# Performance work log

Hardware: AMD Instinct MI355X
Metric: run time of the kernel (lower is better)

Reference implementation:

```python
import jax, jax.numpy as jnp
import numpy as np

WS = 8          # window_size
HEADS = 3       # num_heads
DIM = 96        # dim
PDIM = 30       # GlobalAttention patch_dim
EPS_G = 1e-8    # GlobalAttention eps
ATT_A, ATT_B = 30.0, 20.0


def _rel_pos_log(ws):
    # matches get_relative_positions (torch.meshgrid default 'ij' indexing)
    coords = np.stack(np.meshgrid(np.arange(ws), np.arange(ws), indexing='ij'))  # (2,ws,ws)
    cf = coords.reshape(2, -1)                                                    # (2,N)
    rel = (cf[:, :, None] - cf[:, None, :]).transpose(1, 2, 0).astype(np.float32)  # (N,N,2)
    return jnp.asarray(np.sign(rel) * np.log1p(np.abs(rel)))


def _conv(x, w, stride=1, pad=0, groups=1):
    return jax.lax.conv_general_dilated(
        x, w, (stride, stride), [(pad, pad), (pad, pad)],
        feature_group_count=groups, dimension_numbers=('NCHW', 'OIHW', 'NCHW'))


def _refpad(x, p):
    return jnp.pad(x, ((0, 0), (0, 0), (p, p), (p, p)), mode='reflect')


def _forward(X, hf_w1, hf_b1, hf_w2, hf_b2, lfv_w, lfv_b, lfqk_w, lfqk_b,
             meta_w1, meta_b1, meta_w2, meta_b2,
             pe_w1, pe_b1, pe_w2, pe_b2, att_alpha, att_beta,
             fus_w1, fus_w2):
    B, C, H, W = X.shape
    # ---- high-frequency branch: two depthwise 5x5 convs, reflect padding ----
    hf = _conv(_refpad(X, 2), hf_w1, groups=C) + hf_b1[None, :, None, None]
    hf = jax.nn.relu(hf)
    hf = _conv(_refpad(hf, 2), hf_w2, groups=C) + hf_b2[None, :, None, None]
    # ---- low-frequency branch: build QKV (note torch cat order [QK, V]) ----
    lf_v = _conv(X, lfv_w) + lfv_b[None, :, None, None]
    lf_qk = _conv(X, lfqk_w) + lfqk_b[None, :, None, None]
    qkv = jnp.concatenate([lf_qk, lf_v], axis=1)          # (B,3C,H,W)
    # shift_size=0, H,W divisible by WS -> check_size is identity
    x = qkv.transpose(0, 2, 3, 1)                          # (B,H,W,3C)
    nh, nw = H // WS, W // WS
    N = WS * WS
    win = x.reshape(B, nh, WS, nw, WS, 3 * C).transpose(0, 1, 3, 2, 4, 5)
    win = win.reshape(-1, N, 3 * C)                        # (Bw,N,3C)
    # ---- WindowAttention with MLP relative-position bias ----
    Bw = win.shape[0]
    hd = C // HEADS
    qkv_ = win.reshape(Bw, N, 3, HEADS, hd).transpose(2, 0, 3, 1, 4)
    q = qkv_[0] * (hd ** -0.5)
    k, v = qkv_[1], qkv_[2]
    attn = jnp.einsum('bhnd,bhmd->bhnm', q, k)
    rel = _rel_pos_log(WS)                                 # (N,N,2)
    bias = jax.nn.relu(rel @ meta_w1.T + meta_b1) @ meta_w2.T + meta_b2  # (N,N,heads)
    attn = jax.nn.softmax(attn + bias.transpose(2, 0, 1)[None], axis=-1)
    aw = jnp.einsum('bhnm,bhmd->bhnd', attn, v).transpose(0, 2, 1, 3).reshape(Bw, N, C)
    # ---- GlobalAttention: patch embed, l2norm, exp-similarity, l1norm, AdaIN ----
    x4 = aw.reshape(B, nh, nw, N * C)
    src_mean = x4.mean(axis=(1, 2, 3), keepdims=True)      # (B,1,1,1)
    src_std = jnp.sqrt(((x4 - src_mean) ** 2).mean(axis=(1, 2, 3), keepdims=True) + EPS_G)
    emb = jax.nn.relu(x4 @ pe_w1.T + pe_b1) @ pe_w2.T + pe_b2
    emb = emb.reshape(B, nh * nw, PDIM)
    emb = emb / (jnp.sqrt((emb ** 2).sum(-1, keepdims=True)) + EPS_G)
    att_g = jnp.einsum('bnd,bmd->bnm', emb, emb)           # (B,P,P)
    att_g = jnp.exp(ATT_A * att_alpha[0] * att_g + ATT_B * att_beta[0])
    att_g = att_g / (att_g.sum(-1, keepdims=True) + EPS_G)
    rw = jnp.einsum('bnm,bmc->bnc', att_g, aw.reshape(B, nh * nw, N * C))
    cur_mean = emb.mean(axis=(1, 2), keepdims=True)        # stats of embedded x, per source
    cur_std = jnp.sqrt(((emb - cur_mean) ** 2).mean(axis=(1, 2), keepdims=True) + EPS_G)
    rw = (rw - cur_mean) / cur_std
    rw = rw * src_std[:, :, :, 0] + src_mean[:, :, :, 0]
    # ---- window reverse (shift_size=0 -> slice is identity) ----
    out = rw.reshape(B, nh, nw, WS, WS, C).transpose(0, 1, 3, 2, 4, 5).reshape(B, H, W, C)
    lf = out.transpose(0, 3, 1, 2)                         # (B,C,H,W)
    # ---- SKFusion (keep_dim=True): sum, conv mlp, channel softmax gate ----
    feats_sum = hf + lf
    a = _conv(feats_sum, fus_w1, stride=2, pad=1)
    a = jax.nn.relu(a)
    a = _conv(a, fus_w2, stride=2, pad=1)
    a = a.mean(axis=(2, 3))                                # adaptive avg pool -> (B,C)
    a = jax.nn.softmax(a, axis=1)[:, :, None, None]
    return feats_sum * a


def setup_inputs() -> dict:
    key = jax.random.key(0)
    ks = jax.random.split(key, 24)
    B, C, H, W = 4, DIM, 256, 256
    d_fuse = max(C // 2, 4)
    psrc = WS * WS * C
    s = 0.02
    n = lambda k, sh: jax.random.normal(k, sh, dtype=jnp.float32) * s
    return {
        'X': jax.random.normal(ks[0], (B, C, H, W), dtype=jnp.float32),
        'hf_w1': n(ks[1], (C, 1, 5, 5)), 'hf_b1': n(ks[2], (C,)),
        'hf_w2': n(ks[3], (C, 1, 5, 5)), 'hf_b2': n(ks[4], (C,)),
        'lfv_w': n(ks[5], (C, C, 1, 1)), 'lfv_b': n(ks[6], (C,)),
        'lfqk_w': n(ks[7], (2 * C, C, 1, 1)), 'lfqk_b': n(ks[8], (2 * C,)),
        'meta_w1': n(ks[9], (256, 2)), 'meta_b1': n(ks[10], (256,)),
        'meta_w2': n(ks[11], (HEADS, 256)), 'meta_b2': n(ks[12], (HEADS,)),
        'pe_w1': n(ks[13], (256, psrc)), 'pe_b1': n(ks[14], (256,)),
        'pe_w2': n(ks[15], (PDIM, 256)), 'pe_b2': n(ks[16], (PDIM,)),
        'att_alpha': jax.random.normal(ks[17], (1,), dtype=jnp.float32) * 0.01,
        'att_beta': jax.random.normal(ks[18], (1,), dtype=jnp.float32) * 0.01,
        'fus_w1': n(ks[19], (d_fuse, C, 3, 3)), 'fus_w2': n(ks[20], (C, d_fuse, 3, 3)),
    }


def reference(X, hf_w1, hf_b1, hf_w2, hf_b2, lfv_w, lfv_b, lfqk_w, lfqk_b,
              meta_w1, meta_b1, meta_w2, meta_b2,
              pe_w1, pe_b1, pe_w2, pe_b2, att_alpha, att_beta,
              fus_w1, fus_w2):
    return _forward(X, hf_w1, hf_b1, hf_w2, hf_b2, lfv_w, lfv_b, lfqk_w, lfqk_b,
                    meta_w1, meta_b1, meta_w2, meta_b2,
                    pe_w1, pe_b1, pe_w2, pe_b2, att_alpha, att_beta,
                    fus_w1, fus_w2)
```

## Files before the change

kernel.cpp:

```cpp
#include <hip/hip_runtime.h>

constexpr int B_ = 4, C_ = 96, H_ = 256, W_ = 256;
constexpr int NWINS = 4096;
constexpr float EPSG = 1e-8f;
constexpr float ATT_Ac = 30.f, ATT_Bc = 20.f;
constexpr float QSCALE = 0.17677669529663687f;
constexpr long long BIG = (long long)B_ * C_ * H_ * W_;

typedef unsigned short u16;
typedef unsigned int u32;
typedef __attribute__((ext_vector_type(8))) __bf16 bf16x8;
typedef __attribute__((ext_vector_type(4))) float f32x4;

#define AS(n) __attribute__((address_space(n)))

__device__ __forceinline__ void gload16(const void* g, void* l) {
  __builtin_amdgcn_global_load_lds((AS(1) void*)g, (AS(3) void*)l, 16, 0, 0);
}

__device__ __forceinline__ u16 f2b(float f) {
  union { float f; u32 i; } x; x.f = f;
  u32 r = (x.i + 0x7fffu + ((x.i >> 16) & 1u)) >> 16;
  return (u16)r;
}
__device__ __forceinline__ float blo(u32 u) { union { u32 i; float f; } x; x.i = u << 16; return x.f; }
__device__ __forceinline__ float bhi(u32 u) { union { u32 i; float f; } x; x.i = u & 0xffff0000u; return x.f; }

__global__ void k_wt(const float* __restrict__ lfqk_w, const float* __restrict__ lfqk_b,
                     const float* __restrict__ lfv_w, const float* __restrict__ lfv_b,
                     float* __restrict__ wt, float* __restrict__ bq) {
  int t = blockIdx.x * 256 + threadIdx.x;
  if (t < 96 * 288) {
    int ic = t / 288, oc = t % 288;
    wt[t] = (oc < 192) ? lfqk_w[oc * 96 + ic] : lfv_w[(oc - 192) * 96 + ic];
  }
  if (t < 288) bq[t] = (t < 192) ? lfqk_b[t] : lfv_b[t - 192];
}

__global__ void k_bias(const float* __restrict__ w1, const float* __restrict__ b1,
                       const float* __restrict__ w2, const float* __restrict__ b2,
                       float* __restrict__ bias) {
  int t = blockIdx.x * 256 + threadIdx.x;
  if (t >= 4096) return;
  int n = t >> 6, m = t & 63;
  float dy = (float)((n >> 3) - (m >> 3));
  float dx = (float)((n & 7) - (m & 7));
  float fy = (dy > 0.f ? 1.f : (dy < 0.f ? -1.f : 0.f)) * log1pf(fabsf(dy));
  float fx = (dx > 0.f ? 1.f : (dx < 0.f ? -1.f : 0.f)) * log1pf(fabsf(dx));
  float o0 = b2[0], o1 = b2[1], o2 = b2[2];
  for (int j = 0; j < 256; ++j) {
    float h = fmaxf(w1[2 * j] * fy + w1[2 * j + 1] * fx + b1[j], 0.f);
    o0 += w2[j] * h; o1 += w2[256 + j] * h; o2 += w2[512 + j] * h;
  }
  bias[t] = o0; bias[4096 + t] = o1; bias[8192 + t] = o2;
}

__global__ void k_cvtw(const float* __restrict__ in, u16* __restrict__ out, int n) {
  int i = (blockIdx.x * 256 + threadIdx.x) * 4;
  if (i < n) {
    float4 v = *(const float4*)(in + i);
    out[i] = f2b(v.x); out[i + 1] = f2b(v.y); out[i + 2] = f2b(v.z); out[i + 3] = f2b(v.w);
  }
}

__global__ __launch_bounds__(256) void k_qkv(const float* __restrict__ X,
                      const float* __restrict__ wt, const float* __restrict__ bq,
                      float* __restrict__ q, float* __restrict__ k, float* __restrict__ v) {
  __shared__ float xw[96][64];
  int win = blockIdx.x;
  int b = win >> 10, wy = (win >> 5) & 31, wx = win & 31;
  int t = threadIdx.x;
  const float* Xb = X + (long long)b * 96 * 65536 + wy * 8 * 256 + wx * 8;
  for (int f = t; f < 6144; f += 256) {
    int ic = f >> 6, p = f & 63;
    xw[ic][p] = Xb[ic * 65536 + (p >> 3) * 256 + (p & 7)];
  }
  __syncthreads();
  int lane = t & 63, quad = t >> 6;
  int nbase = quad * 16;
  for (int ob = 0; ob < 288; ob += 64) {
    int oc = ob + lane;
    if (oc < 288) {
      float acc[16];
#pragma unroll
      for (int i = 0; i < 16; ++i) acc[i] = 0.f;
#pragma unroll 4
      for (int ic = 0; ic < 96; ++ic) {
        float wv = wt[ic * 288 + oc];
        const float4* xr = (const float4*)&xw[ic][nbase];
#pragma unroll
        for (int g = 0; g < 4; ++g) {
          float4 x = xr[g];
          acc[4 * g + 0] += wv * x.x; acc[4 * g + 1] += wv * x.y;
          acc[4 * g + 2] += wv * x.z; acc[4 * g + 3] += wv * x.w;
        }
      }
      float bb = bq[oc];
      int s = oc / 96, c = oc % 96;
      float scale = (s == 0) ? QSCALE : 1.f;
      float* dst = ((s == 0) ? q : (s == 1) ? k : v) + (long long)win * 6144 + c;
#pragma unroll
      for (int i = 0; i < 16; ++i) dst[(nbase + i) * 96] = (acc[i] + bb) * scale;
    }
  }
}

__global__ __launch_bounds__(192) void k_attn(const float* __restrict__ q, const float* __restrict__ kk_,
                       const float* __restrict__ v, const float* __restrict__ bias,
                       u16* __restrict__ awB) {
  __shared__ float kl[3][64][32];
  __shared__ float vl[3][64][32];
  int win = blockIdx.x;
  int t = threadIdx.x;
  long long base = (long long)win * 6144;
  for (int f = t; f < 6144; f += 192) {
    int n = f / 96, c = f % 96, h = c >> 5, d = c & 31;
    kl[h][n][d] = kk_[base + f];
    vl[h][n][d] = v[base + f];
  }
  __syncthreads();
  int h = t >> 6, lane = t & 63;
  float qr[32];
  const float4* qp = (const float4*)(q + base + lane * 96 + h * 32);
#pragma unroll
  for (int i = 0; i < 8; ++i) {
    float4 x = qp[i];
    qr[4 * i] = x.x; qr[4 * i + 1] = x.y; qr[4 * i + 2] = x.z; qr[4 * i + 3] = x.w;
  }
  const float* bh = bias + h * 4096 + lane * 64;
  float s[64];
#pragma unroll
  for (int m = 0; m < 64; ++m) {
    float acc = 0.f;
    const float4* kp = (const float4*)kl[h][m];
#pragma unroll
    for (int i = 0; i < 8; ++i) {
      float4 x = kp[i];
      acc += qr[4 * i] * x.x + qr[4 * i + 1] * x.y + qr[4 * i + 2] * x.z + qr[4 * i + 3] * x.w;
    }
    s[m] = acc + bh[m];
  }
  float mx = -1e30f;
#pragma unroll
  for (int m = 0; m < 64; ++m) mx = fmaxf(mx, s[m]);
  float sum = 0.f;
#pragma unroll
  for (int m = 0; m < 64; ++m) { float p = __expf(s[m] - mx); s[m] = p; sum += p; }
  float inv = 1.f / sum;
  float o[32];
#pragma unroll
  for (int d = 0; d < 32; ++d) o[d] = 0.f;
#pragma unroll
  for (int m = 0; m < 64; ++m) {
    float p = s[m];
    const float4* vp = (const float4*)vl[h][m];
#pragma unroll
    for (int i = 0; i < 8; ++i) {
      float4 x = vp[i];
      o[4 * i] += p * x.x; o[4 * i + 1] += p * x.y; o[4 * i + 2] += p * x.z; o[4 * i + 3] += p * x.w;
    }
  }
  u32 pk[16];
#pragma unroll
  for (int j = 0; j < 16; ++j)
    pk[j] = (u32)f2b(o[2 * j] * inv) | ((u32)f2b(o[2 * j + 1] * inv) << 16);
  u32* op = (u32*)(awB + base + lane * 96 + h * 32);
#pragma unroll
  for (int j = 0; j < 16; ++j) op[j] = pk[j];
}

__global__ __launch_bounds__(256) void k_awT(const u16* __restrict__ awB, u16* __restrict__ awT) {
  __shared__ u16 tile[64][80];
  int f0 = blockIdx.x * 64, p0 = blockIdx.y * 64, b = blockIdx.z;
  int t = threadIdx.x;
  const u16* src = awB + ((long long)b * 1024 + p0) * 6144 + f0;
  int pr = t >> 2, fc = (t & 3) * 16;
  uint4 v0 = *(const uint4*)(src + (long long)pr * 6144 + fc);
  uint4 v1 = *(const uint4*)(src + (long long)pr * 6144 + fc + 8);
  u16 e[16];
  *(uint4*)&e[0] = v0; *(uint4*)&e[8] = v1;
#pragma unroll
  for (int j = 0; j < 16; ++j) tile[fc + j][pr] = e[j];
  __syncthreads();
  int fr = t >> 2, pc = (t & 3) * 16;
  u16* dst = awT + ((long long)b * 6144 + f0 + fr) * 1024 + p0 + pc;
  *(uint4*)(dst) = *(const uint4*)&tile[fr][pc];
  *(uint4*)(dst + 8) = *(const uint4*)&tile[fr][pc + 8];
}

__global__ void k_redA(const u16* __restrict__ awB, float* __restrict__ part) {
  int b = blockIdx.x, blk = blockIdx.y, t = threadIdx.x;
  const uint4* p = (const uint4*)(awB + (long long)b * 6291456 + (long long)blk * 49152);
  float s = 0.f, ss = 0.f;
  for (int i = t; i < 6144; i += 256) {
    uint4 x = p[i];
    u32 w[4] = {x.x, x.y, x.z, x.w};
#pragma unroll
    for (int j = 0; j < 4; ++j) {
      float a = blo(w[j]), c = bhi(w[j]);
      s += a + c; ss += a * a + c * c;
    }
  }
  __shared__ float r1[256], r2[256];
  r1[t] = s; r2[t] = ss; __syncthreads();
  for (int st = 128; st; st >>= 1) {
    if (t < st) { r1[t] += r1[t + st]; r2[t] += r2[t + st]; }
    __syncthreads();
  }
  if (t == 0) { part[(b * 128 + blk) * 2] = r1[0]; part[(b * 128 + blk) * 2 + 1] = r2[0]; }
}

__global__ void k_redB(const float* __restrict__ part, float* __restrict__ stats) {
  int b = blockIdx.x, t = threadIdx.x;
  float s = part[(b * 128 + t) * 2], ss = part[(b * 128 + t) * 2 + 1];
  __shared__ float r1[128], r2[128];
  r1[t] = s; r2[t] = ss; __syncthreads();
  for (int st = 64; st; st >>= 1) {
    if (t < st) { r1[t] += r1[t + st]; r2[t] += r2[t + st]; }
    __syncthreads();
  }
  if (t == 0) {
    float n = 6291456.f, m = r1[0] / n;
    stats[b] = m;
    stats[4 + b] = sqrtf(fmaxf(r2[0] / n - m * m, 0.f) + EPSG);
  }
}

__global__ __launch_bounds__(256) void k_embed1(const u16* __restrict__ awB, const u16* __restrict__ peB,
                         const float* __restrict__ b1, float* __restrict__ hid) {
  __shared__ __align__(16) u16 As[128 * 32];
  __shared__ __align__(16) u16 Bs[64 * 32];
  int n0 = blockIdx.x * 64, m0 = blockIdx.y * 128;
  int t = threadIdx.x;
  const u16* Ag = awB + (long long)m0 * 6144;
  const u16* Bg = peB + (long long)n0 * 6144;
  f32x4 acc[4][2];
  f32x4 z = {0.f, 0.f, 0.f, 0.f};
#pragma unroll
  for (int i = 0; i < 4; ++i) { acc[i][0] = z; acc[i][1] = z; }
  int w = t >> 6, l = t & 63;
  int wm = (w >> 1) * 64, wn = (w & 1) * 32;
  int ro = l & 15, ko = (l >> 4) * 16;
  for (int k0 = 0; k0 < 6144; k0 += 32) {
#pragma unroll
    for (int i = 0; i < 2; ++i) {
      int c = t + 256 * i;
      gload16(Ag + (long long)(c >> 2) * 6144 + k0 + (c & 3) * 8, (char*)As + c * 16);
    }
    gload16(Bg + (long long)(t >> 2) * 6144 + k0 + (t & 3) * 8, (char*)Bs + t * 16);
    __syncthreads();
    bf16x8 a[4], bb[2];
#pragma unroll
    for (int fm = 0; fm < 4; ++fm)
      a[fm] = *(const bf16x8*)((const char*)As + (wm + fm * 16 + ro) * 64 + ko);
#pragma unroll
    for (int fn = 0; fn < 2; ++fn)
      bb[fn] = *(const bf16x8*)((const char*)Bs + (wn + fn * 16 + ro) * 64 + ko);
#pragma unroll
    for (int fm = 0; fm < 4; ++fm)
#pragma unroll
      for (int fn = 0; fn < 2; ++fn)
        acc[fm][fn] = __builtin_amdgcn_mfma_f32_16x16x32_bf16(a[fm], bb[fn], acc[fm][fn], 0, 0, 0);
    __syncthreads();
  }
#pragma unroll
  for (int fm = 0; fm < 4; ++fm)
#pragma unroll
    for (int r = 0; r < 4; ++r) {
      int m = m0 + wm + fm * 16 + (l >> 4) * 4 + r;
#pragma unroll
      for (int fn = 0; fn < 2; ++fn) {
        int n = n0 + wn + fn * 16 + (l & 15);
        hid[(long long)m * 256 + n] = fmaxf(acc[fm][fn][r] + b1[n], 0.f);
      }
    }
}

__global__ __launch_bounds__(64) void k_embed2(const float* __restrict__ hid, const float* __restrict__ w2,
                        const float* __restrict__ b2, float* __restrict__ emb) {
  __shared__ float hrow[256];
  int pa = blockIdx.x, t = threadIdx.x;
  const float* hp = hid + (long long)pa * 256;
  for (int i = t; i < 256; i += 64) hrow[i] = hp[i];
  __syncthreads();
  float acc = 0.f;
  if (t < 30) {
    acc = b2[t];
    const float* wp = w2 + t * 256;
    for (int j = 0; j < 256; ++j) acc += wp[j] * hrow[j];
  }
  float sq = (t < 30) ? acc * acc : 0.f;
  for (int off = 32; off; off >>= 1) sq += __shfl_down(sq, off);
  float ss = __shfl(sq, 0);
  float scale = 1.f / (sqrtf(ss) + EPSG);
  if (t < 30) emb[(long long)pa * 30 + t] = acc * scale;
}

__global__ void k_curstats(const float* __restrict__ emb, float* __restrict__ stats) {
  int b = blockIdx.x, t = threadIdx.x;
  const float* p = emb + (long long)b * 30720;
  float s = 0.f, ss = 0.f;
  for (int i = t; i < 30720; i += 256) { float x = p[i]; s += x; ss += x * x; }
  __shared__ float r1[256], r2[256];
  r1[t] = s; r2[t] = ss; __syncthreads();
  for (int st = 128; st; st >>= 1) {
    if (t < st) { r1[t] += r1[t + st]; r2[t] += r2[t + st]; }
    __syncthreads();
  }
  if (t == 0) {
    float n = 30720.f, m = r1[0] / n;
    stats[8 + b] = m;
    stats[12 + b] = sqrtf(fmaxf(r2[0] / n - m * m, 0.f) + EPSG);
  }
}

__global__ void k_gatt(const float* __restrict__ emb, const float* __restrict__ alpha,
                       const float* __restrict__ beta, u16* __restrict__ attB) {
  __shared__ float er[64][33];
  __shared__ float ec[64][33];
  int b = blockIdx.x, r0 = blockIdx.y * 64, t = threadIdx.x;
  const float* eb = emb + (long long)b * 30720;
  for (int f = t; f < 1920; f += 256) er[f / 30][f % 30] = eb[(r0 + f / 30) * 30 + f % 30];
  float ca = ATT_Ac * alpha[0], cb = ATT_Bc * beta[0];
  int lane = t & 63, w = t >> 6;
  for (int c0 = 0; c0 < 1024; c0 += 64) {
    __syncthreads();
    for (int f = t; f < 1920; f += 256) ec[f / 30][f % 30] = eb[(c0 + f / 30) * 30 + f % 30];
    __syncthreads();
    for (int rr = w; rr < 64; rr += 4) {
      float acc = 0.f;
#pragma unroll
      for (int d = 0; d < 30; ++d) acc += er[rr][d] * ec[lane][d];
      attB[((long long)b * 1024 + r0 + rr) * 1024 + c0 + lane] = f2b(__expf(ca * acc + cb));
    }
  }
}

__global__ void k_rowsum(const u16* __restrict__ attB, float* __restrict__ rowsum) {
  int row = blockIdx.x * 4 + (threadIdx.x >> 6);
  int lane = threadIdx.x & 63;
  const uint4* p = (const uint4*)(attB + (long long)row * 1024);
  float s = 0.f;
  for (int i = lane; i < 128; i += 64) {
    uint4 x = p[i];
    s += blo(x.x) + bhi(x.x) + blo(x.y) + bhi(x.y) + blo(x.z) + bhi(x.z) + blo(x.w) + bhi(x.w);
  }
  for (int off = 32; off; off >>= 1) s += __shfl_down(s, off);
  if (lane == 0) rowsum[row] = s;
}

__global__ __launch_bounds__(256) void k_rw(const u16* __restrict__ attB, const u16* __restrict__ x4T,
                     const float* __restrict__ rowsum, const float* __restrict__ stats,
                     float* __restrict__ rw) {
  __shared__ __align__(16) u16 As[128 * 32];
  __shared__ __align__(16) u16 Bs[128 * 32];
  int b = blockIdx.z;
  int n0 = blockIdx.x * 128, m0 = blockIdx.y * 128;
  const u16* Ag = attB + ((long long)b * 1024 + m0) * 1024;
  const u16* Bg = x4T + ((long long)b * 6144 + n0) * 1024;
  int t = threadIdx.x;
  f32x4 acc[4][4];
  f32x4 z = {0.f, 0.f, 0.f, 0.f};
#pragma unroll
  for (int i = 0; i < 4; ++i)
#pragma unroll
    for (int j = 0; j < 4; ++j) acc[i][j] = z;
  int w = t >> 6, l = t & 63;
  int wm = (w >> 1) * 64, wn = (w & 1) * 64;
  int ro = l & 15, ko = (l >> 4) * 16;
  for (int k0 = 0; k0 < 1024; k0 += 32) {
#pragma unroll
    for (int i = 0; i < 2; ++i) {
      int c = t + 256 * i;
      gload16(Ag + (c >> 2) * 1024 + k0 + (c & 3) * 8, (char*)As + c * 16);
      gload16(Bg + (c >> 2) * 1024 + k0 + (c & 3) * 8, (char*)Bs + c * 16);
    }
    __syncthreads();
    bf16x8 a[4], bb[4];
#pragma unroll
    for (int fm = 0; fm < 4; ++fm)
      a[fm] = *(const bf16x8*)((const char*)As + (wm + fm * 16 + ro) * 64 + ko);
#pragma unroll
    for (int fn = 0; fn < 4; ++fn)
      bb[fn] = *(const bf16x8*)((const char*)Bs + (wn + fn * 16 + ro) * 64 + ko);
#pragma unroll
    for (int fm = 0; fm < 4; ++fm)
#pragma unroll
      for (int fn = 0; fn < 4; ++fn)
        acc[fm][fn] = __builtin_amdgcn_mfma_f32_16x16x32_bf16(a[fm], bb[fn], acc[fm][fn], 0, 0, 0);
    __syncthreads();
  }
  float sm = stats[b], ssd = stats[4 + b], cm = stats[8 + b], inv_cs = 1.f / stats[12 + b];
#pragma unroll
  for (int fm = 0; fm < 4; ++fm)
#pragma unroll
    for (int r = 0; r < 4; ++r) {
      int m = m0 + wm + fm * 16 + (l >> 4) * 4 + r;
      float sc = 1.f / (rowsum[b * 1024 + m] + EPSG);
      float* dst = rw + ((long long)b * 1024 + m) * 6144 + n0 + wn + (l & 15);
#pragma unroll
      for (int fn = 0; fn < 4; ++fn) {
        float val = acc[fm][fn][r] * sc;
        dst[fn * 16] = (val - cm) * inv_cs * ssd + sm;
      }
    }
}

template <bool RELU>
__global__ void k_dwconv(const float* __restrict__ in, const float* __restrict__ w,
                         const float* __restrict__ bias, float* __restrict__ out) {
  int x = blockIdx.x * 64 + threadIdx.x;
  int y = blockIdx.y * 4 + threadIdx.y;
  int bc = blockIdx.z, c = bc % 96;
  const float* ip = in + (long long)bc * 65536;
  const float* wp = w + c * 25;
  float acc = bias[c];
#pragma unroll
  for (int ky = 0; ky < 5; ++ky) {
    int iy = y + ky - 2;
    iy = iy < 0 ? -iy : (iy > 255 ? 510 - iy : iy);
    const float* row = ip + iy * 256;
#pragma unroll
    for (int kx = 0; kx < 5; ++kx) {
      int ix = x + kx - 2;
      ix = ix < 0 ? -ix : (ix > 255 ? 510 - ix : ix);
      acc += wp[ky * 5 + kx] * row[ix];
    }
  }
  out[(long long)bc * 65536 + y * 256 + x] = RELU ? fmaxf(acc, 0.f) : acc;
}

__global__ void k_fs(const float* __restrict__ rw, const float* __restrict__ hf,
                     float* __restrict__ fs) {
  __shared__ float tile[64 * 97];
  int win = blockIdx.x;
  int b = win >> 10, wy = (win >> 5) & 31, wx = win & 31;
  int t = threadIdx.x;
  const float* src = rw + (long long)win * 6144;
  for (int f = t; f < 6144; f += 256) tile[(f / 96) * 97 + f % 96] = src[f];
  __syncthreads();
  long long obase = (long long)b * 96 * 65536;
  for (int f = t; f < 6144; f += 256) {
    int c = f >> 6, p = f & 63;
    long long oidx = obase + (long long)c * 65536 + (wy * 8 + (p >> 3)) * 256 + wx * 8 + (p & 7);
    fs[oidx] = tile[p * 97 + c] + hf[oidx];
  }
}

__global__ void k_conv1(const float* __restrict__ fs, const float* __restrict__ w,
                        float* __restrict__ out) {
  int ox = blockIdx.x * 64 + threadIdx.x;
  int oy = blockIdx.y * 4 + threadIdx.y;
  int z = blockIdx.z, b = z / 6, og = z % 6, oc0 = og * 8;
  const float* ip = fs + (long long)b * 96 * 65536;
  float acc[8] = {};
  for (int ic = 0; ic < 96; ++ic) {
    const float* plane = ip + (long long)ic * 65536;
    float xv[3][3];
#pragma unroll
    for (int ky = 0; ky < 3; ++ky) {
      int iy = 2 * oy + ky - 1;
#pragma unroll
      for (int kx = 0; kx < 3; ++kx) {
        int ix = 2 * ox + kx - 1;
        xv[ky][kx] = (iy >= 0 && iy < 256 && ix >= 0 && ix < 256) ? plane[iy * 256 + ix] : 0.f;
      }
    }
#pragma unroll
    for (int o = 0; o < 8; ++o) {
      const float* wp = w + ((oc0 + o) * 96 + ic) * 9;
      acc[o] += wp[0] * xv[0][0] + wp[1] * xv[0][1] + wp[2] * xv[0][2]
              + wp[3] * xv[1][0] + wp[4] * xv[1][1] + wp[5] * xv[1][2]
              + wp[6] * xv[2][0] + wp[7] * xv[2][1] + wp[8] * xv[2][2];
    }
  }
#pragma unroll
  for (int o = 0; o < 8; ++o)
    out[(((long long)b * 48 + oc0 + o) * 128 + oy) * 128 + ox] = fmaxf(acc[o], 0.f);
}

__global__ void k_conv2pool(const float* __restrict__ c1, const float* __restrict__ w,
                            float* __restrict__ part) {
  int b = blockIdx.x, og = blockIdx.y, split = blockIdx.z, oc0 = og * 8;
  int t = threadIdx.x;
  const float* ip = c1 + (long long)b * 48 * 16384;
  float acc[8] = {};
  for (int pi = 0; pi < 2; ++pi) {
    int p = split * 512 + pi * 256 + t;
    int oy = p >> 6, ox = p & 63;
    for (int ic = 0; ic < 48; ++ic) {
      const float* plane = ip + ic * 16384;
      float xv[3][3];
#pragma unroll
      for (int ky = 0; ky < 3; ++ky) {
        int iy = 2 * oy + ky - 1;
#pragma unroll
        for (int kx = 0; kx < 3; ++kx) {
          int ix = 2 * ox + kx - 1;
          xv[ky][kx] = (iy >= 0 && iy < 128 && ix >= 0 && ix < 128) ? plane[iy * 128 + ix] : 0.f;
        }
      }
#pragma unroll
      for (int o = 0; o < 8; ++o) {
        const float* wp = w + ((oc0 + o) * 48 + ic) * 9;
        acc[o] += wp[0] * xv[0][0] + wp[1] * xv[0][1] + wp[2] * xv[0][2]
                + wp[3] * xv[1][0] + wp[4] * xv[1][1] + wp[5] * xv[1][2]
                + wp[6] * xv[2][0] + wp[7] * xv[2][1] + wp[8] * xv[2][2];
      }
    }
  }
  __shared__ float red[256];
  for (int o = 0; o < 8; ++o) {
    red[t] = acc[o]; __syncthreads();
    for (int st = 128; st; st >>= 1) {
      if (t < st) red[t] += red[t + st];
      __syncthreads();
    }
    if (t == 0) part[((b * 12 + og) * 8 + split) * 8 + o] = red[0];
    __syncthreads();
  }
}

__global__ void k_gate(const float* __restrict__ part, float* __restrict__ gate) {
  int b = blockIdx.x, t = threadIdx.x;
  __shared__ float val[96];
  __shared__ float red[128];
  if (t < 96) {
    int og = t / 8, o = t % 8;
    float s = 0.f;
    for (int sp = 0; sp < 8; ++sp) s += part[((b * 12 + og) * 8 + sp) * 8 + o];
    val[t] = s / 4096.f;
  }
  __syncthreads();
  float m = (t < 96) ? val[t] : -1e30f;
  red[t] = m; __syncthreads();
  for (int st = 64; st; st >>= 1) { if (t < st) red[t] = fmaxf(red[t], red[t + st]); __syncthreads(); }
  float mx = red[0]; __syncthreads();
  float e = (t < 96) ? __expf(val[t] - mx) : 0.f;
  red[t] = e; __syncthreads();
  for (int st = 64; st; st >>= 1) { if (t < st) red[t] += red[t + st]; __syncthreads(); }
  if (t < 96) gate[b * 96 + t] = e / red[0];
}

__global__ void k_final(const float* __restrict__ fs, const float* __restrict__ gate,
                        float* __restrict__ out) {
  long long i0 = ((long long)blockIdx.x * 256 + threadIdx.x) * 4;
  long long stride = (long long)gridDim.x * 1024;
  for (long long i = i0; i < 25165824LL; i += stride) {
    float4 x = *(const float4*)(fs + i);
    float g = gate[(int)(i >> 16)];
    x.x *= g; x.y *= g; x.z *= g; x.w *= g;
    *(float4*)(out + i) = x;
  }
}

extern "C" void kernel_launch(void* const* d_in, const int* in_sizes, int n_in,
                              void* d_out, int out_size, void* d_ws, size_t ws_size,
                              hipStream_t stream) {
  const float* X      = (const float*)d_in[0];
  const float* hf_w1  = (const float*)d_in[1];
  const float* hf_b1  = (const float*)d_in[2];
  const float* hf_w2  = (const float*)d_in[3];
  const float* hf_b2  = (const float*)d_in[4];
  const float* lfv_w  = (const float*)d_in[5];
  const float* lfv_b  = (const float*)d_in[6];
  const float* lfqk_w = (const float*)d_in[7];
  const float* lfqk_b = (const float*)d_in[8];
  const float* mw1    = (const float*)d_in[9];
  const float* mb1    = (const float*)d_in[10];
  const float* mw2    = (const float*)d_in[11];
  const float* mb2    = (const float*)d_in[12];
  const float* pe_w1  = (const float*)d_in[13];
  const float* pe_b1  = (const float*)d_in[14];
  const float* pe_w2  = (const float*)d_in[15];
  const float* pe_b2  = (const float*)d_in[16];
  const float* aalpha = (const float*)d_in[17];
  const float* abeta  = (const float*)d_in[18];
  const float* fus_w1 = (const float*)d_in[19];
  const float* fus_w2 = (const float*)d_in[20];

  float* W = (float*)d_ws;
  float* q    = W;
  float* kbuf = W + BIG;
  u16* awB = (u16*)(W + 2 * BIG);
  u16* awT = awB + BIG;
  float* rw  = W;
  float* hf1 = W + BIG;
  float* fs  = W + 2 * BIG;
  float* SM = W + 3 * BIG;
  float* bias_tab  = SM;
  float* wt        = SM + 12288;
  float* bqv       = SM + 39936;
  float* hid       = SM + 40224;
  float* emb       = SM + 1088800;
  u16*   attB      = (u16*)(SM + 1211680);
  float* rowsum    = SM + 3308832;
  float* part_src  = SM + 3312928;
  float* stats     = SM + 3313952;
  float* part_pool = SM + 3313968;
  float* gate      = SM + 3317040;
  float* c1        = SM + 3317424;
  u16*   peB       = (u16*)(SM + 6463152);
  float* v  = (float*)d_out;
  float* hf = (float*)d_out;

  k_wt<<<108, 256, 0, stream>>>(lfqk_w, lfqk_b, lfv_w, lfv_b, wt, bqv);
  k_bias<<<16, 256, 0, stream>>>(mw1, mb1, mw2, mb2, bias_tab);
  k_cvtw<<<1536, 256, 0, stream>>>(pe_w1, peB, 256 * 6144);
  k_qkv<<<NWINS, 256, 0, stream>>>(X, wt, bqv, q, kbuf, v);
  k_attn<<<NWINS, 192, 0, stream>>>(q, kbuf, v, bias_tab, awB);
  k_awT<<<dim3(96, 16, 4), 256, 0, stream>>>(awB, awT);
  k_redA<<<dim3(4, 128), 256, 0, stream>>>(awB, part_src);
  k_redB<<<4, 128, 0, stream>>>(part_src, stats);
  k_embed1<<<dim3(4, 32), 256, 0, stream>>>(awB, peB, pe_b1, hid);
  k_embed2<<<4096, 64, 0, stream>>>(hid, pe_w2, pe_b2, emb);
  k_curstats<<<4, 256, 0, stream>>>(emb, stats);
  k_gatt<<<dim3(4, 16), 256, 0, stream>>>(emb, aalpha, abeta, attB);
  k_rowsum<<<1024, 256, 0, stream>>>(attB, rowsum);
  k_rw<<<dim3(48, 8, 4), 256, 0, stream>>>(attB, awT, rowsum, stats, rw);
  k_dwconv<true><<<dim3(4, 64, 384), dim3(64, 4), 0, stream>>>(X, hf_w1, hf_b1, hf1);
  k_dwconv<false><<<dim3(4, 64, 384), dim3(64, 4), 0, stream>>>(hf1, hf_w2, hf_b2, hf);
  k_fs<<<NWINS, 256, 0, stream>>>(rw, hf, fs);
  k_conv1<<<dim3(2, 32, 24), dim3(64, 4), 0, stream>>>(fs, fus_w1, c1);
  k_conv2pool<<<dim3(4, 12, 8), 256, 0, stream>>>(c1, fus_w2, part_pool);
  k_gate<<<4, 128, 0, stream>>>(part_pool, gate);
  k_final<<<2048, 256, 0, stream>>>(fs, gate, (float*)d_out);
}
```

Before: 1.900 ms.

## Fuse QKV projection and window attention into one MFMA bf16 kernel

Replaces the separate fp32 QKV 1x1-conv kernel and fp32 window-attention kernel with a single per-window kernel. It computes QKV with bf16 MFMA from pre-swizzled weight fragments and keeps Q/K/V in swizzled LDS. QK^T, softmax and PV then run on MFMA inside the same block. This removes the fp32 q/k/v round trip through global memory and the scalar FMA loops, at the cost of bf16 rounding of X, the weights, the QKV values and the probabilities.

```diff
diff --git a/kernel.cpp b/kernel.cpp
--- a/kernel.cpp
+++ b/kernel.cpp
@@ -25,14 +25,20 @@
 }
 __device__ __forceinline__ float blo(u32 u) { union { u32 i; float f; } x; x.i = u << 16; return x.f; }
 __device__ __forceinline__ float bhi(u32 u) { union { u32 i; float f; } x; x.i = u & 0xffff0000u; return x.f; }
-
-__global__ void k_wt(const float* __restrict__ lfqk_w, const float* __restrict__ lfqk_b,
-                     const float* __restrict__ lfv_w, const float* __restrict__ lfv_b,
-                     float* __restrict__ wt, float* __restrict__ bq) {
+__device__ __forceinline__ __bf16 f2bf(float f) { union { u16 u; __bf16 b; } c; c.u = f2b(f); return c.b; }
+
+__global__ void k_wt2(const float* __restrict__ lfqk_w, const float* __restrict__ lfqk_b,
+                      const float* __restrict__ lfv_w, const float* __restrict__ lfv_b,
+                      u16* __restrict__ wfrag, float* __restrict__ bq) {
   int t = blockIdx.x * 256 + threadIdx.x;
-  if (t < 96 * 288) {
-    int ic = t / 288, oc = t % 288;
-    wt[t] = (oc < 192) ? lfqk_w[oc * 96 + ic] : lfv_w[(oc - 192) * 96 + ic];
+  if (t < 27648) {
+    int ot = t / 1536, r1 = t % 1536;
+    int ks = r1 / 512, q = r1 % 512;
+    int l = q >> 3, j = q & 7;
+    int oc = ot * 16 + (l & 15);
+    int ic = ks * 32 + (l >> 4) * 8 + j;
+    float wv = (oc < 192) ? lfqk_w[oc * 96 + ic] : lfv_w[(oc - 192) * 96 + ic];
+    wfrag[t] = f2b(wv);
   }
   if (t < 288) bq[t] = (t < 192) ? lfqk_b[t] : lfv_b[t - 192];
 }
@@ -63,110 +69,138 @@
   }
 }
 
-__global__ __launch_bounds__(256) void k_qkv(const float* __restrict__ X,
-                      const float* __restrict__ wt, const float* __restrict__ bq,
-                      float* __restrict__ q, float* __restrict__ k, float* __restrict__ v) {
-  __shared__ float xw[96][64];
+__global__ __launch_bounds__(256) void k_front(const float* __restrict__ X,
+                       const u16* __restrict__ wfrag, const float* __restrict__ bqv,
+                       const float* __restrict__ bias_tab, u16* __restrict__ awB) {
+  __shared__ u16 uni[3][4096];
+  __shared__ u16 vt[3][2048];
   int win = blockIdx.x;
   int b = win >> 10, wy = (win >> 5) & 31, wx = win & 31;
   int t = threadIdx.x;
-  const float* Xb = X + (long long)b * 96 * 65536 + wy * 8 * 256 + wx * 8;
-  for (int f = t; f < 6144; f += 256) {
-    int ic = f >> 6, p = f & 63;
-    xw[ic][p] = Xb[ic * 65536 + (p >> 3) * 256 + (p & 7)];
+  int w = t >> 6, l = t & 63;
+  int lr = l & 15, lg = l >> 4;
+  int p = w * 16 + lr;
+  const float* Xp = X + (long long)b * 96 * 65536 + (wy * 8 + (p >> 3)) * 256 + wx * 8 + (p & 7);
+  bf16x8 xf[3];
+#pragma unroll
+  for (int ks = 0; ks < 3; ++ks)
+#pragma unroll
+    for (int j = 0; j < 8; ++j)
+      xf[ks][j] = f2bf(Xp[(ks * 32 + lg * 8 + j) * 65536]);
+  f32x4 acc[18];
+  f32x4 z = {0.f, 0.f, 0.f, 0.f};
+#pragma unroll
+  for (int ot = 0; ot < 18; ++ot) acc[ot] = z;
+#pragma unroll
+  for (int ks = 0; ks < 3; ++ks)
+#pragma unroll
+    for (int ot = 0; ot < 18; ++ot) {
+      bf16x8 af = *(const bf16x8*)(wfrag + ((ot * 3 + ks) * 64 + l) * 8);
+      acc[ot] = __builtin_amdgcn_mfma_f32_16x16x32_bf16(af, xf[ks], acc[ot], 0, 0, 0);
+    }
+#pragma unroll
+  for (int ot = 0; ot < 18; ++ot) {
+#pragma unroll
+    for (int r = 0; r < 4; ++r) {
+      int oc = ot * 16 + lg * 4 + r;
+      float vv = acc[ot][r] + bqv[oc];
+      int s3 = ot / 6;
+      int cc = oc - s3 * 96, h = cc >> 5, d = cc & 31;
+      if (s3 == 0) vv *= QSCALE;
+      u16 bv = f2b(vv);
+      if (s3 < 2) {
+        int byo = s3 * 4096 + (((p * 64 + 2 * d) ^ ((p & 3) << 4)));
+        *(u16*)((char*)uni[h] + byo) = bv;
+      } else {
+        int byo = (d * 128 + 2 * p) ^ ((d & 7) << 4);
+        *(u16*)((char*)vt[h] + byo) = bv;
+      }
+    }
   }
   __syncthreads();
-  int lane = t & 63, quad = t >> 6;
-  int nbase = quad * 16;
-  for (int ob = 0; ob < 288; ob += 64) {
-    int oc = ob + lane;
-    if (oc < 288) {
-      float acc[16];
-#pragma unroll
-      for (int i = 0; i < 16; ++i) acc[i] = 0.f;
-#pragma unroll 4
-      for (int ic = 0; ic < 96; ++ic) {
-        float wv = wt[ic * 288 + oc];
-        const float4* xr = (const float4*)&xw[ic][nbase];
-#pragma unroll
-        for (int g = 0; g < 4; ++g) {
-          float4 x = xr[g];
-          acc[4 * g + 0] += wv * x.x; acc[4 * g + 1] += wv * x.y;
-          acc[4 * g + 2] += wv * x.z; acc[4 * g + 3] += wv * x.w;
+  if (w < 3) {
+    int h = w;
+    bf16x8 qf[4], kf[4];
+#pragma unroll
+    for (int qt = 0; qt < 4; ++qt) {
+      int row = qt * 16 + lr;
+      qf[qt] = *(const bf16x8*)((char*)uni[h] + (((row * 64 + lg * 16) ^ ((row & 3) << 4))));
+      kf[qt] = *(const bf16x8*)((char*)uni[h] + 4096 + (((row * 64 + lg * 16) ^ ((row & 3) << 4))));
+    }
+    f32x4 s[4][4];
+#pragma unroll
+    for (int qt = 0; qt < 4; ++qt)
+#pragma unroll
+      for (int kt = 0; kt < 4; ++kt)
+        s[qt][kt] = __builtin_amdgcn_mfma_f32_16x16x32_bf16(qf[qt], kf[kt], z, 0, 0, 0);
+    const float* bt = bias_tab + h * 4096;
+#pragma unroll
+    for (int qt = 0; qt < 4; ++qt)
+#pragma unroll
+      for (int r = 0; r < 4; ++r) {
+        int n = qt * 16 + lg * 4 + r;
+#pragma unroll
+        for (int kt = 0; kt < 4; ++kt)
+          s[qt][kt][r] += bt[n * 64 + kt * 16 + lr];
+      }
+#pragma unroll
+    for (int qt = 0; qt < 4; ++qt)
+#pragma unroll
+      for (int r = 0; r < 4; ++r) {
+        float m = fmaxf(fmaxf(s[qt][0][r], s[qt][1][r]), fmaxf(s[qt][2][r], s[qt][3][r]));
+        m = fmaxf(m, __shfl_xor(m, 1)); m = fmaxf(m, __shfl_xor(m, 2));
+        m = fmaxf(m, __shfl_xor(m, 4)); m = fmaxf(m, __shfl_xor(m, 8));
+        float sum = 0.f;
+#pragma unroll
+        for (int kt = 0; kt < 4; ++kt) {
+          float e = __expf(s[qt][kt][r] - m);
+          s[qt][kt][r] = e; sum += e;
         }
-      }
-      float bb = bq[oc];
-      int s = oc / 96, c = oc % 96;
-      float scale = (s == 0) ? QSCALE : 1.f;
-      float* dst = ((s == 0) ? q : (s == 1) ? k : v) + (long long)win * 6144 + c;
-#pragma unroll
-      for (int i = 0; i < 16; ++i) dst[(nbase + i) * 96] = (acc[i] + bb) * scale;
-    }
-  }
-}
-
-__global__ __launch_bounds__(192) void k_attn(const float* __restrict__ q, const float* __restrict__ kk_,
-                       const float* __restrict__ v, const float* __restrict__ bias,
-                       u16* __restrict__ awB) {
-  __shared__ float kl[3][64][32];
-  __shared__ float vl[3][64][32];
-  int win = blockIdx.x;
-  int t = threadIdx.x;
-  long long base = (long long)win * 6144;
-  for (int f = t; f < 6144; f += 192) {
-    int n = f / 96, c = f % 96, h = c >> 5, d = c & 31;
-    kl[h][n][d] = kk_[base + f];
-    vl[h][n][d] = v[base + f];
-  }
-  __syncthreads();
-  int h = t >> 6, lane = t & 63;
-  float qr[32];
-  const float4* qp = (const float4*)(q + base + lane * 96 + h * 32);
-#pragma unroll
-  for (int i = 0; i < 8; ++i) {
-    float4 x = qp[i];
-    qr[4 * i] = x.x; qr[4 * i + 1] = x.y; qr[4 * i + 2] = x.z; qr[4 * i + 3] = x.w;
-  }
-  const float* bh = bias + h * 4096 + lane * 64;
-  float s[64];
-#pragma unroll
-  for (int m = 0; m < 64; ++m) {
-    float acc = 0.f;
-    const float4* kp = (const float4*)kl[h][m];
-#pragma unroll
-    for (int i = 0; i < 8; ++i) {
-      float4 x = kp[i];
-      acc += qr[4 * i] * x.x + qr[4 * i + 1] * x.y + qr[4 * i + 2] * x.z + qr[4 * i + 3] * x.w;
-    }
-    s[m] = acc + bh[m];
-  }
-  float mx = -1e30f;
-#pragma unroll
-  for (int m = 0; m < 64; ++m) mx = fmaxf(mx, s[m]);
-  float sum = 0.f;
-#pragma unroll
-  for (int m = 0; m < 64; ++m) { float p = __expf(s[m] - mx); s[m] = p; sum += p; }
-  float inv = 1.f / sum;
-  float o[32];
-#pragma unroll
-  for (int d = 0; d < 32; ++d) o[d] = 0.f;
-#pragma unroll
-  for (int m = 0; m < 64; ++m) {
-    float p = s[m];
-    const float4* vp = (const float4*)vl[h][m];
-#pragma unroll
-    for (int i = 0; i < 8; ++i) {
-      float4 x = vp[i];
-      o[4 * i] += p * x.x; o[4 * i + 1] += p * x.y; o[4 * i + 2] += p * x.z; o[4 * i + 3] += p * x.w;
-    }
-  }
-  u32 pk[16];
-#pragma unroll
-  for (int j = 0; j < 16; ++j)
-    pk[j] = (u32)f2b(o[2 * j] * inv) | ((u32)f2b(o[2 * j + 1] * inv) << 16);
-  u32* op = (u32*)(awB + base + lane * 96 + h * 32);
-#pragma unroll
-  for (int j = 0; j < 16; ++j) op[j] = pk[j];
+        sum += __shfl_xor(sum, 1); sum += __shfl_xor(sum, 2);
+        sum += __shfl_xor(sum, 4); sum += __shfl_xor(sum, 8);
+        float inv = 1.f / sum;
+        int q = qt * 16 + lg * 4 + r;
+#pragma unroll
+        for (int kt = 0; kt < 4; ++kt) {
+          int kp = kt * 16 + lr;
+          int byo = (q * 128 + 2 * kp) ^ ((q & 7) << 4);
+          *(u16*)((char*)uni[h] + byo) = f2b(s[qt][kt][r] * inv);
+        }
+      }
+    f32x4 o[4][2];
+#pragma unroll
+    for (int qt = 0; qt < 4; ++qt) { o[qt][0] = z; o[qt][1] = z; }
+#pragma unroll
+    for (int kv = 0; kv < 2; ++kv) {
+      bf16x8 ap[4], bv[2];
+#pragma unroll
+      for (int qt = 0; qt < 4; ++qt) {
+        int q = qt * 16 + lr;
+        ap[qt] = *(const bf16x8*)((char*)uni[h] + (((q * 128 + kv * 64 + lg * 16) ^ ((q & 7) << 4))));
+      }
+#pragma unroll
+      for (int dt = 0; dt < 2; ++dt) {
+        int d = dt * 16 + lr;
+        bv[dt] = *(const bf16x8*)((char*)vt[h] + (((d * 128 + kv * 64 + lg * 16) ^ ((d & 7) << 4))));
+      }
+#pragma unroll
+      for (int qt = 0; qt < 4; ++qt)
+#pragma unroll
+        for (int dt = 0; dt < 2; ++dt)
+          o[qt][dt] = __builtin_amdgcn_mfma_f32_16x16x32_bf16(ap[qt], bv[dt], o[qt][dt], 0, 0, 0);
+    }
+    u16* ob = awB + (long long)win * 6144;
+#pragma unroll
+    for (int qt = 0; qt < 4; ++qt)
+#pragma unroll
+      for (int dt = 0; dt < 2; ++dt)
+#pragma unroll
+        for (int r = 0; r < 4; ++r) {
+          int q = qt * 16 + lg * 4 + r;
+          int c = h * 32 + dt * 16 + lr;
+          ob[q * 96 + c] = f2b(o[qt][dt][r]);
+        }
+  }
 }
 
 __global__ __launch_bounds__(256) void k_awT(const u16* __restrict__ awB, u16* __restrict__ awT) {
@@ -580,35 +614,31 @@
   const float* fus_w2 = (const float*)d_in[20];
 
   float* W = (float*)d_ws;
-  float* q    = W;
-  float* kbuf = W + BIG;
+  float* rw  = W;
+  float* hf1 = W + BIG;
   u16* awB = (u16*)(W + 2 * BIG);
   u16* awT = awB + BIG;
-  float* rw  = W;
-  float* hf1 = W + BIG;
   float* fs  = W + 2 * BIG;
   float* SM = W + 3 * BIG;
   float* bias_tab  = SM;
-  float* wt        = SM + 12288;
-  float* bqv       = SM + 39936;
-  float* hid       = SM + 40224;
-  float* emb       = SM + 1088800;
-  u16*   attB      = (u16*)(SM + 1211680);
-  float* rowsum    = SM + 3308832;
-  float* part_src  = SM + 3312928;
-  float* stats     = SM + 3313952;
-  float* part_pool = SM + 3313968;
-  float* gate      = SM + 3317040;
-  float* c1        = SM + 3317424;
-  u16*   peB       = (u16*)(SM + 6463152);
-  float* v  = (float*)d_out;
+  u16*   wfrag     = (u16*)(SM + 12288);
+  float* bqv       = SM + 26112;
+  float* hid       = SM + 26400;
+  float* emb       = SM + 1074976;
+  u16*   attB      = (u16*)(SM + 1197856);
+  float* rowsum    = SM + 3295008;
+  float* part_src  = SM + 3299104;
+  float* stats     = SM + 3300128;
+  float* part_pool = SM + 3300144;
+  float* gate      = SM + 3303216;
+  float* c1        = SM + 3303600;
+  u16*   peB       = (u16*)(SM + 6449328);
   float* hf = (float*)d_out;
 
-  k_wt<<<108, 256, 0, stream>>>(lfqk_w, lfqk_b, lfv_w, lfv_b, wt, bqv);
+  k_wt2<<<108, 256, 0, stream>>>(lfqk_w, lfqk_b, lfv_w, lfv_b, wfrag, bqv);
   k_bias<<<16, 256, 0, stream>>>(mw1, mb1, mw2, mb2, bias_tab);
   k_cvtw<<<1536, 256, 0, stream>>>(pe_w1, peB, 256 * 6144);
-  k_qkv<<<NWINS, 256, 0, stream>>>(X, wt, bqv, q, kbuf, v);
-  k_attn<<<NWINS, 192, 0, stream>>>(q, kbuf, v, bias_tab, awB);
+  k_front<<<NWINS, 256, 0, stream>>>(X, wfrag, bqv, bias_tab, awB);
   k_awT<<<dim3(96, 16, 4), 256, 0, stream>>>(awB, awT);
   k_redA<<<dim3(4, 128), 256, 0, stream>>>(awB, part_src);
   k_redB<<<4, 128, 0, stream>>>(part_src, stats);
```

Measured after the change: 1.545 ms. -18.7%, faster.
